# Kernel optimization log

Measured on AMD Instinct MI355X. Metric: run time of the kernel, lower is better.

Reference implementation:

```python
import jax, jax.numpy as jnp
import numpy as np

B = 8          # number of subgraphs (seq_start_end rows)
N = 2048       # nodes per subgraph (equal-size segments)
D = 64         # h_dim
H = 4          # gat_heads
ALPHA = 0.2    # leaky relu slope


def setup_inputs() -> dict:
    key = jax.random.key(0)
    k1, k2, k3, k4, k5 = jax.random.split(key, 5)
    h_states = jax.random.normal(k1, (B * N, D), dtype=jnp.float32)
    # xavier-ish scales
    W_heads = jax.random.normal(k2, (H, D, D), dtype=jnp.float32) * (1.414 * np.sqrt(2.0 / (D + D)))
    a_heads = jax.random.normal(k3, (H, 2 * D), dtype=jnp.float32) * (1.414 * np.sqrt(2.0 / (2 * D + 1)))
    W_out = jax.random.normal(k4, (H * D, D), dtype=jnp.float32) * (1.414 * np.sqrt(2.0 / (H * D + D)))
    a_out = jax.random.normal(k5, (2 * D,), dtype=jnp.float32) * (1.414 * np.sqrt(2.0 / (2 * D + 1)))
    starts = jnp.arange(B, dtype=jnp.int32) * N
    seq_start_end = jnp.stack([starts, starts + N], axis=1)  # (B, 2)
    return {"h_states": h_states, "W_heads": W_heads, "a_heads": a_heads,
            "W_out": W_out, "a_out": a_out, "seq_start_end": seq_start_end}


def _gat_layer(x, W, a):
    """Dense GAT layer. Equivalent to the torch.cat O(N^2*2d) construction,
    rewritten as separate a1/a2 projections + broadcast add. Eval mode (no dropout)."""
    h = x @ W                      # (N, dout)
    d = W.shape[1]
    s1 = h @ a[:d]                 # (N,)  score contribution of source node i
    s2 = h @ a[d:]                 # (N,)  score contribution of target node j
    e = jax.nn.leaky_relu(s1[:, None] + s2[None, :], ALPHA)  # (N, N)
    attn = jax.nn.softmax(e, axis=1)
    return attn @ h                # (N, dout)


def reference(h_states, W_heads, a_heads, W_out, a_out, seq_start_end):
    # seq_start_end encodes B equal contiguous segments of length N -> reshape
    x = h_states.reshape(B, N, D)

    def per_graph(xg):  # xg: (N, D)
        # multi-head attention layers, concat=True -> elu on each head output
        hp = jax.vmap(lambda W, a: jax.nn.elu(_gat_layer(xg, W, a)))(W_heads, a_heads)  # (H, N, D)
        xc = jnp.transpose(hp, (1, 0, 2)).reshape(N, H * D)
        # output attention layer, concat=False (no elu inside), then elu + log_softmax outside
        out = jax.nn.elu(_gat_layer(xc, W_out, a_out))   # (N, D)
        return jax.nn.log_softmax(out, axis=1)

    return jax.vmap(per_graph)(x).reshape(B * N, D)
```

## Files before the change

### kernel.cpp

```cpp
#include <hip/hip_runtime.h>
#include <math.h>

#define NTOT 16384
#define NSEG 2048
#define TROW 65
#define TSTRIDE 133185ull

#define OFF_HH   0ull
#define OFF_XC   4194304ull
#define OFF_S1H  8388608ull
#define OFF_S2H  8454144ull
#define OFF_S1O  8519680ull
#define OFF_S2O  8536064ull
#define OFF_SVAL 8552448ull
#define OFF_WN   8617984ull
#define OFF_CHA  8683520ull
#define OFF_CHS  8949760ull
#define OFF_SIDX 9216000ull
#define OFF_A    9281536ull
#define OFF_S    13543456ull

__device__ inline unsigned long long pack_key(float v, int idx) {
    unsigned u = __float_as_uint(v);
    u = (u & 0x80000000u) ? ~u : (u | 0x80000000u);
    return ((unsigned long long)u << 32) | (unsigned)idx;
}
__device__ inline float unpack_key(unsigned long long k) {
    unsigned u = (unsigned)(k >> 32);
    u = (u & 0x80000000u) ? (u ^ 0x80000000u) : ~u;
    return __uint_as_float(u);
}
__device__ inline unsigned long long shfl_xor_u64(unsigned long long x, int mask) {
    unsigned lo = (unsigned)x, hi = (unsigned)(x >> 32);
    lo = (unsigned)__shfl_xor((int)lo, mask, 64);
    hi = (unsigned)__shfl_xor((int)hi, mask, 64);
    return ((unsigned long long)hi << 32) | lo;
}

__global__ __launch_bounds__(256) void gemm1_k(const float* __restrict__ X,
                                               const float* __restrict__ Wh,
                                               const float* __restrict__ aH,
                                               float* __restrict__ hh,
                                               float* __restrict__ s1h,
                                               float* __restrict__ s2h) {
    __shared__ float As[64][68];
    __shared__ float Bs[64][68];
    const int tid = threadIdx.x;
    const int bm = blockIdx.x, h = blockIdx.y;
    const int c0 = tid & 63, r0 = tid >> 6;
#pragma unroll
    for (int r = 0; r < 16; ++r) {
        int row = r0 + r * 4;
        As[c0][row] = X[(size_t)(bm * 64 + row) * 64 + c0];
        Bs[row][c0] = Wh[h * 4096 + row * 64 + c0];
    }
    __syncthreads();
    const int tx = tid & 15, ty = tid >> 4;
    const int m0 = ty * 4, n0 = tx * 4;
    float acc[4][4] = {};
#pragma unroll
    for (int kk = 0; kk < 64; ++kk) {
        float4 a = *(const float4*)&As[kk][m0];
        float4 b = *(const float4*)&Bs[kk][n0];
        acc[0][0] += a.x * b.x; acc[0][1] += a.x * b.y; acc[0][2] += a.x * b.z; acc[0][3] += a.x * b.w;
        acc[1][0] += a.y * b.x; acc[1][1] += a.y * b.y; acc[1][2] += a.y * b.z; acc[1][3] += a.y * b.w;
        acc[2][0] += a.z * b.x; acc[2][1] += a.z * b.y; acc[2][2] += a.z * b.z; acc[2][3] += a.z * b.w;
        acc[3][0] += a.w * b.x; acc[3][1] += a.w * b.y; acc[3][2] += a.w * b.z; acc[3][3] += a.w * b.w;
    }
#pragma unroll
    for (int i = 0; i < 4; ++i) {
        float4 v = make_float4(acc[i][0], acc[i][1], acc[i][2], acc[i][3]);
        *(float4*)&hh[(size_t)(bm * 64 + m0 + i) * 256 + h * 64 + n0] = v;
    }
#pragma unroll
    for (int i = 0; i < 4; ++i) {
        float p1 = 0.f, p2 = 0.f;
#pragma unroll
        for (int jj = 0; jj < 4; ++jj) {
            p1 += acc[i][jj] * aH[h * 128 + n0 + jj];
            p2 += acc[i][jj] * aH[h * 128 + 64 + n0 + jj];
        }
#pragma unroll
        for (int off = 8; off; off >>= 1) {
            p1 += __shfl_xor(p1, off, 16);
            p2 += __shfl_xor(p2, off, 16);
        }
        if (tx == 0) {
            s1h[h * NTOT + bm * 64 + m0 + i] = p1;
            s2h[h * NTOT + bm * 64 + m0 + i] = p2;
        }
    }
}

__global__ __launch_bounds__(256) void gemm2_k(const float* __restrict__ XC,
                                               const float* __restrict__ Wo,
                                               const float* __restrict__ aO,
                                               float* __restrict__ hc,
                                               float* __restrict__ s1o,
                                               float* __restrict__ s2o) {
    __shared__ float As[64][68];
    __shared__ float Bs[64][68];
    const int tid = threadIdx.x;
    const int bm = blockIdx.x;
    const int c0 = tid & 63, r0 = tid >> 6;
    const int tx = tid & 15, ty = tid >> 4;
    const int m0 = ty * 4, n0 = tx * 4;
    float acc[4][4] = {};
    for (int kt = 0; kt < 4; ++kt) {
#pragma unroll
        for (int r = 0; r < 16; ++r) {
            int row = r0 + r * 4;
            As[c0][row] = XC[(size_t)(bm * 64 + row) * 256 + kt * 64 + c0];
            Bs[row][c0] = Wo[(kt * 64 + row) * 64 + c0];
        }
        __syncthreads();
#pragma unroll
        for (int kk = 0; kk < 64; ++kk) {
            float4 a = *(const float4*)&As[kk][m0];
            float4 b = *(const float4*)&Bs[kk][n0];
            acc[0][0] += a.x * b.x; acc[0][1] += a.x * b.y; acc[0][2] += a.x * b.z; acc[0][3] += a.x * b.w;
            acc[1][0] += a.y * b.x; acc[1][1] += a.y * b.y; acc[1][2] += a.y * b.z; acc[1][3] += a.y * b.w;
            acc[2][0] += a.z * b.x; acc[2][1] += a.z * b.y; acc[2][2] += a.z * b.z; acc[2][3] += a.z * b.w;
            acc[3][0] += a.w * b.x; acc[3][1] += a.w * b.y; acc[3][2] += a.w * b.z; acc[3][3] += a.w * b.w;
        }
        __syncthreads();
    }
#pragma unroll
    for (int i = 0; i < 4; ++i) {
        float4 v = make_float4(acc[i][0], acc[i][1], acc[i][2], acc[i][3]);
        *(float4*)&hc[(size_t)(bm * 64 + m0 + i) * 64 + n0] = v;
    }
#pragma unroll
    for (int i = 0; i < 4; ++i) {
        float p1 = 0.f, p2 = 0.f;
#pragma unroll
        for (int jj = 0; jj < 4; ++jj) {
            p1 += acc[i][jj] * aO[n0 + jj];
            p2 += acc[i][jj] * aO[64 + n0 + jj];
        }
#pragma unroll
        for (int off = 8; off; off >>= 1) {
            p1 += __shfl_xor(p1, off, 16);
            p2 += __shfl_xor(p2, off, 16);
        }
        if (tx == 0) {
            s1o[bm * 64 + m0 + i] = p1;
            s2o[bm * 64 + m0 + i] = p2;
        }
    }
}

__global__ __launch_bounds__(1024) void sort_k(const float* __restrict__ s2_all, int heads,
                                               float* __restrict__ g_sval, int* __restrict__ g_sidx,
                                               float* __restrict__ g_wN) {
    __shared__ unsigned long long sA[1024];
    __shared__ unsigned long long sB[1024];
    __shared__ float sM2;
    const int tid = threadIdx.x, t = blockIdx.x;
    const int g = t / heads, h = t % heads;
    const float* s2p = s2_all + (size_t)h * NTOT + (size_t)g * NSEG;
    unsigned long long a0 = pack_key(s2p[tid], tid);
    unsigned long long a1 = pack_key(s2p[tid + 1024], tid + 1024);
    for (int k = 2; k <= 2048; k <<= 1) {
        const bool up0 = (tid & k) == 0;
        const bool up1 = (((tid + 1024) & k) == 0);
        for (int j = k >> 1; j > 0; j >>= 1) {
            if (j >= 1024) {
                unsigned long long lo = a0 < a1 ? a0 : a1;
                unsigned long long hi = a0 < a1 ? a1 : a0;
                a0 = up0 ? lo : hi;
                a1 = up0 ? hi : lo;
            } else if (j >= 64) {
                __syncthreads();
                sA[tid] = a0; sB[tid] = a1;
                __syncthreads();
                unsigned long long p0 = sA[tid ^ j], p1 = sB[tid ^ j];
                bool lower = (tid & j) == 0;
                a0 = ((a0 < p0) == (lower == up0)) ? a0 : p0;
                a1 = ((a1 < p1) == (lower == up1)) ? a1 : p1;
            } else {
                unsigned long long p0 = shfl_xor_u64(a0, j);
                unsigned long long p1 = shfl_xor_u64(a1, j);
                bool lower = (tid & j) == 0;
                a0 = ((a0 < p0) == (lower == up0)) ? a0 : p0;
                a1 = ((a1 < p1) == (lower == up1)) ? a1 : p1;
            }
        }
    }
    float v0 = unpack_key(a0), v1 = unpack_key(a1);
    if (tid == 1023) sM2 = v1;
    __syncthreads();
    const float M2 = sM2;
    size_t o = (size_t)t * NSEG;
    g_sval[o + tid] = v0;
    g_sval[o + tid + 1024] = v1;
    g_sidx[o + tid] = (int)(unsigned)(a0 & 0xffffffffu);
    g_sidx[o + tid + 1024] = (int)(unsigned)(a1 & 0xffffffffu);
    g_wN[o + tid] = __expf(0.2f * (v0 - M2));
    g_wN[o + tid + 1024] = __expf(0.2f * (v1 - M2));
}

__global__ __launch_bounds__(256) void chunks_k(const float* __restrict__ V,
                                                int heads, int vstride,
                                                const int* __restrict__ g_sidx,
                                                const float* __restrict__ g_wN,
                                                float* __restrict__ g_chA, float* __restrict__ g_chS) {
    const int t = blockIdx.y, g = t / heads, h = t % heads;
    const int wv = threadIdx.x >> 6, lane = threadIdx.x & 63;
    const int c = blockIdx.x * 4 + wv, base = c * 16;
    const float* Vp = V + (size_t)g * NSEG * vstride + h * 64;
    float wn_l = 0.f; int si_l = 0;
    if (lane < 16) {
        wn_l = g_wN[(size_t)t * NSEG + base + lane];
        si_l = g_sidx[(size_t)t * NSEG + base + lane];
    }
    float sa = 0.f, swa = 0.f, ss = 0.f, sws = 0.f;
#pragma unroll
    for (int j = 0; j < 16; ++j) {
        float wn = __shfl(wn_l, j, 64);
        int row = __shfl(si_l, j, 64);
        float v = Vp[(size_t)row * vstride + lane];
        float w2 = wn * wn, wp = w2 * w2 * wn;
        sa += wn * v; swa += wn;
        ss += wp * v; sws += wp;
    }
    size_t o = ((size_t)t * 128 + c) * TROW;
    g_chA[o + lane] = sa;
    g_chS[o + lane] = ss;
    if (lane == 0) { g_chA[o + 64] = swa; g_chS[o + 64] = sws; }
}

__global__ __launch_bounds__(256) void scan_k(float* __restrict__ g_chA, float* __restrict__ g_chS,
                                              float* __restrict__ g_A, float* __restrict__ g_S) {
    __shared__ float M[128 * 65];
    const int t = blockIdx.x, tid = threadIdx.x;
    for (int i = tid; i < 8320; i += 256) M[i] = g_chA[(size_t)t * 8320 + i];
    __syncthreads();
    if (tid < 65) {
        float run = 0.f;
        for (int c = 0; c < 128; ++c) { float v = M[c * 65 + tid]; M[c * 65 + tid] = run; run += v; }
        g_A[(size_t)t * TSTRIDE + (size_t)2048 * TROW + tid] = run;
    }
    __syncthreads();
    for (int i = tid; i < 8320; i += 256) g_chA[(size_t)t * 8320 + i] = M[i];
    __syncthreads();
    for (int i = tid; i < 8320; i += 256) M[i] = g_chS[(size_t)t * 8320 + i];
    __syncthreads();
    if (tid < 65) {
        float run = 0.f;
        for (int c = 127; c >= 0; --c) { run += M[c * 65 + tid]; M[c * 65 + tid] = run; }
        g_S[(size_t)t * TSTRIDE + (size_t)2048 * TROW + tid] = 0.f;
    }
    __syncthreads();
    for (int i = tid; i < 8320; i += 256) g_chS[(size_t)t * 8320 + i] = M[i];
}

__global__ __launch_bounds__(256) void seg_tab_k(const float* __restrict__ V,
                                                 int heads, int vstride,
                                                 const int* __restrict__ g_sidx,
                                                 const float* __restrict__ g_wN,
                                                 const float* __restrict__ g_chA,
                                                 const float* __restrict__ g_chS,
                                                 float* __restrict__ g_A, float* __restrict__ g_S) {
    const int t = blockIdx.y, g = t / heads, h = t % heads;
    const int wv = threadIdx.x >> 6, lane = threadIdx.x & 63;
    const int c = blockIdx.x * 4 + wv;
    const int base = c * 16;
    const float* Vp = V + (size_t)g * NSEG * vstride + h * 64;
    const int* sidx = g_sidx + (size_t)t * NSEG + base;
    const float* wnp = g_wN + (size_t)t * NSEG + base;
    float wn[16], vv[16];
#pragma unroll
    for (int j = 0; j < 16; ++j) wn[j] = wnp[j];
#pragma unroll
    for (int j = 0; j < 16; ++j) vv[j] = Vp[(size_t)sidx[j] * vstride + lane];
    float* A = g_A + (size_t)t * TSTRIDE;
    float* S = g_S + (size_t)t * TSTRIDE;
    float accA = g_chA[((size_t)t * 128 + c) * TROW + lane];
    float scaA = g_chA[((size_t)t * 128 + c) * TROW + 64];
#pragma unroll
    for (int j = 0; j < 16; ++j) {
        size_t pos = base + j;
        A[pos * TROW + lane] = accA;
        if (lane == 0) A[pos * TROW + 64] = scaA;
        accA += wn[j] * vv[j]; scaA += wn[j];
    }
    float accS = 0.f, scaS = 0.f;
    if (c < 127) {
        accS = g_chS[((size_t)t * 128 + c + 1) * TROW + lane];
        scaS = g_chS[((size_t)t * 128 + c + 1) * TROW + 64];
    }
#pragma unroll
    for (int j = 15; j >= 0; --j) {
        float w = wn[j], w2 = w * w, wp = w2 * w2 * w;
        accS += wp * vv[j]; scaS += wp;
        size_t pos = base + j;
        S[pos * TROW + lane] = accS;
        if (lane == 0) S[pos * TROW + 64] = scaS;
    }
}

template <int MODE>
__global__ __launch_bounds__(256) void seg_query_k(const float* __restrict__ s1_all,
                                                   float* __restrict__ out,
                                                   int heads, int ostride,
                                                   const float* __restrict__ g_sval,
                                                   const float* __restrict__ g_A,
                                                   const float* __restrict__ g_S) {
    __shared__ float sval[NSEG];
    const int tid = threadIdx.x;
    const int t = blockIdx.y, g = t / heads, h = t % heads;
    const float4* sv4 = (const float4*)(g_sval + (size_t)t * NSEG);
    for (int i = tid; i < NSEG / 4; i += 256) ((float4*)sval)[i] = sv4[i];
    __syncthreads();
    const float M2 = sval[NSEG - 1];
    const int lane = tid & 63, wv = tid >> 6;
    const int q0 = blockIdx.x * 128 + wv * 32;
    const float* s1p = s1_all + (size_t)h * NTOT + (size_t)g * NSEG;
    float* outp = out + (size_t)g * NSEG * ostride + h * 64;
    const float* A = g_A + (size_t)t * TSTRIDE;
    const float* S = g_S + (size_t)t * TSTRIDE;
    int myq = q0 + (lane & 31);
    float s1v = s1p[myq];
    float th = -s1v;
    int lo = 0, hi = NSEG;
    while (lo < hi) { int mid = (lo + hi) >> 1; if (sval[mid] <= th) lo = mid + 1; else hi = mid; }
    for (int j = 0; j < 32; ++j) {
        int k = __shfl(lo, j, 64);
        float s1q = __shfl(s1v, j, 64);
        const float* rowA = A + (size_t)k * TROW;
        const float* rowS = S + (size_t)k * TROW;
        float accA = rowA[lane], scaA = rowA[64];
        float accS = rowS[lane], scaS = rowS[64];
        float cc = __expf(-0.8f * fmaxf(s1q + M2, 0.f));
        float o = (accS + cc * accA) / (scaS + cc * scaA);
        o = o > 0.f ? o : expm1f(o);
        int q = q0 + j;
        if (MODE == 0) {
            outp[(size_t)q * ostride + lane] = o;
        } else {
            float m = o;
#pragma unroll
            for (int off = 32; off; off >>= 1) m = fmaxf(m, __shfl_xor(m, off, 64));
            float e = __expf(o - m);
#pragma unroll
            for (int off = 32; off; off >>= 1) e += __shfl_xor(e, off, 64);
            outp[(size_t)q * ostride + lane] = o - m - __logf(e);
        }
    }
}

extern "C" void kernel_launch(void* const* d_in, const int* in_sizes, int n_in,
                              void* d_out, int out_size, void* d_ws, size_t ws_size,
                              hipStream_t stream) {
    const float* h_states = (const float*)d_in[0];
    const float* W_heads = (const float*)d_in[1];
    const float* a_heads = (const float*)d_in[2];
    const float* W_out = (const float*)d_in[3];
    const float* a_out = (const float*)d_in[4];
    float* w = (float*)d_ws;
    float* hh = w + OFF_HH;
    float* xc = w + OFF_XC;
    float* hc = w + OFF_HH;
    float* s1h = w + OFF_S1H;
    float* s2h = w + OFF_S2H;
    float* s1o = w + OFF_S1O;
    float* s2o = w + OFF_S2O;
    float* g_sval = w + OFF_SVAL;
    float* g_wN = w + OFF_WN;
    float* g_chA = w + OFF_CHA;
    float* g_chS = w + OFF_CHS;
    int* g_sidx = (int*)(w + OFF_SIDX);
    float* g_A = w + OFF_A;
    float* g_S = w + OFF_S;
    float* outp = (float*)d_out;

    gemm1_k<<<dim3(256, 4), 256, 0, stream>>>(h_states, W_heads, a_heads, hh, s1h, s2h);
    sort_k<<<32, 1024, 0, stream>>>(s2h, 4, g_sval, g_sidx, g_wN);
    chunks_k<<<dim3(32, 32), 256, 0, stream>>>(hh, 4, 256, g_sidx, g_wN, g_chA, g_chS);
    scan_k<<<32, 256, 0, stream>>>(g_chA, g_chS, g_A, g_S);
    seg_tab_k<<<dim3(32, 32), 256, 0, stream>>>(hh, 4, 256, g_sidx, g_wN, g_chA, g_chS, g_A, g_S);
    seg_query_k<0><<<dim3(16, 32), 256, 0, stream>>>(s1h, xc, 4, 256, g_sval, g_A, g_S);
    gemm2_k<<<256, 256, 0, stream>>>(xc, W_out, a_out, hc, s1o, s2o);
    sort_k<<<8, 1024, 0, stream>>>(s2o, 1, g_sval, g_sidx, g_wN);
    chunks_k<<<dim3(32, 8), 256, 0, stream>>>(hc, 1, 64, g_sidx, g_wN, g_chA, g_chS);
    scan_k<<<8, 256, 0, stream>>>(g_chA, g_chS, g_A, g_S);
    seg_tab_k<<<dim3(32, 8), 256, 0, stream>>>(hc, 1, 64, g_sidx, g_wN, g_chA, g_chS, g_A, g_S);
    seg_query_k<1><<<dim3(16, 8), 256, 0, stream>>>(s1o, outp, 1, 64, g_sval, g_A, g_S);
}
```

Measured before the change: 211.4 us.

## Fuse sort, chunk reduction and scan into one kernel; halve queries per block

Merges the bitonic sort, the per-chunk weighted sums and the chunk prefix scan into a single 1024-thread block per (graph, head). Sorted indices and weights stay in shared memory, and the scan runs as a two-level blocked scan in LDS. This removes two kernel launches and a global round trip of the chunk tables. The trade-off is only 32 (or 8) blocks doing the chunk gathers, which lowers parallelism for that phase. Separately, the query kernel now handles 16 queries per wave instead of 32 with twice as many blocks, to raise occupancy.

```diff
diff --git a/kernel.cpp b/kernel.cpp
--- a/kernel.cpp
+++ b/kernel.cpp
@@ -150,15 +150,27 @@
     }
 }
 
-__global__ __launch_bounds__(1024) void sort_k(const float* __restrict__ s2_all, int heads,
-                                               float* __restrict__ g_sval, int* __restrict__ g_sidx,
-                                               float* __restrict__ g_wN) {
+__global__ __launch_bounds__(1024) void sortchunkscan_k(const float* __restrict__ s2_all,
+                                                        const float* __restrict__ V,
+                                                        int heads, int vstride,
+                                                        float* __restrict__ g_sval, int* __restrict__ g_sidx,
+                                                        float* __restrict__ g_wN,
+                                                        float* __restrict__ g_chA, float* __restrict__ g_chS,
+                                                        float* __restrict__ g_A, float* __restrict__ g_S) {
     __shared__ unsigned long long sA[1024];
     __shared__ unsigned long long sB[1024];
+    __shared__ float chA[8320];
+    __shared__ float chS[8320];
+    __shared__ float swn[NSEG];
+    __shared__ int ssi[NSEG];
+    __shared__ float btA[4][65];
+    __shared__ float btS[4][65];
     __shared__ float sM2;
     const int tid = threadIdx.x, t = blockIdx.x;
     const int g = t / heads, h = t % heads;
     const float* s2p = s2_all + (size_t)h * NTOT + (size_t)g * NSEG;
+    const float* Vp = V + (size_t)g * NSEG * vstride + h * 64;
+
     unsigned long long a0 = pack_key(s2p[tid], tid);
     unsigned long long a1 = pack_key(s2p[tid + 1024], tid + 1024);
     for (int k = 2; k <= 2048; k <<= 1) {
@@ -191,68 +203,68 @@
     if (tid == 1023) sM2 = v1;
     __syncthreads();
     const float M2 = sM2;
+    int i0 = (int)(unsigned)(a0 & 0xffffffffu);
+    int i1 = (int)(unsigned)(a1 & 0xffffffffu);
+    float w0 = __expf(0.2f * (v0 - M2));
+    float w1 = __expf(0.2f * (v1 - M2));
     size_t o = (size_t)t * NSEG;
-    g_sval[o + tid] = v0;
-    g_sval[o + tid + 1024] = v1;
-    g_sidx[o + tid] = (int)(unsigned)(a0 & 0xffffffffu);
-    g_sidx[o + tid + 1024] = (int)(unsigned)(a1 & 0xffffffffu);
-    g_wN[o + tid] = __expf(0.2f * (v0 - M2));
-    g_wN[o + tid + 1024] = __expf(0.2f * (v1 - M2));
-}
-
-__global__ __launch_bounds__(256) void chunks_k(const float* __restrict__ V,
-                                                int heads, int vstride,
-                                                const int* __restrict__ g_sidx,
-                                                const float* __restrict__ g_wN,
-                                                float* __restrict__ g_chA, float* __restrict__ g_chS) {
-    const int t = blockIdx.y, g = t / heads, h = t % heads;
-    const int wv = threadIdx.x >> 6, lane = threadIdx.x & 63;
-    const int c = blockIdx.x * 4 + wv, base = c * 16;
-    const float* Vp = V + (size_t)g * NSEG * vstride + h * 64;
-    float wn_l = 0.f; int si_l = 0;
-    if (lane < 16) {
-        wn_l = g_wN[(size_t)t * NSEG + base + lane];
-        si_l = g_sidx[(size_t)t * NSEG + base + lane];
-    }
-    float sa = 0.f, swa = 0.f, ss = 0.f, sws = 0.f;
-#pragma unroll
-    for (int j = 0; j < 16; ++j) {
-        float wn = __shfl(wn_l, j, 64);
-        int row = __shfl(si_l, j, 64);
-        float v = Vp[(size_t)row * vstride + lane];
-        float w2 = wn * wn, wp = w2 * w2 * wn;
-        sa += wn * v; swa += wn;
-        ss += wp * v; sws += wp;
-    }
-    size_t o = ((size_t)t * 128 + c) * TROW;
-    g_chA[o + lane] = sa;
-    g_chS[o + lane] = ss;
-    if (lane == 0) { g_chA[o + 64] = swa; g_chS[o + 64] = sws; }
-}
-
-__global__ __launch_bounds__(256) void scan_k(float* __restrict__ g_chA, float* __restrict__ g_chS,
-                                              float* __restrict__ g_A, float* __restrict__ g_S) {
-    __shared__ float M[128 * 65];
-    const int t = blockIdx.x, tid = threadIdx.x;
-    for (int i = tid; i < 8320; i += 256) M[i] = g_chA[(size_t)t * 8320 + i];
+    g_sval[o + tid] = v0; g_sval[o + tid + 1024] = v1;
+    g_sidx[o + tid] = i0; g_sidx[o + tid + 1024] = i1;
+    g_wN[o + tid] = w0;   g_wN[o + tid + 1024] = w1;
+    swn[tid] = w0; swn[tid + 1024] = w1;
+    ssi[tid] = i0; ssi[tid + 1024] = i1;
+    __syncthreads();
+    const int wv = tid >> 6, lane = tid & 63;
+    for (int cc = 0; cc < 8; ++cc) {
+        int c = wv * 8 + cc, base = c * 16;
+        float sa = 0.f, swa = 0.f, ss = 0.f, sws = 0.f;
+#pragma unroll
+        for (int j = 0; j < 16; ++j) {
+            float wn = swn[base + j];
+            int row = ssi[base + j];
+            float v = Vp[(size_t)row * vstride + lane];
+            float w2 = wn * wn, wp = w2 * w2 * wn;
+            sa += wn * v; swa += wn;
+            ss += wp * v; sws += wp;
+        }
+        chA[c * 65 + lane] = sa; chS[c * 65 + lane] = ss;
+        if (lane == 0) { chA[c * 65 + 64] = swa; chS[c * 65 + 64] = sws; }
+    }
+    __syncthreads();
+    if (tid < 260) {
+        int b = tid / 65, d = tid % 65;
+        float run = 0.f;
+        for (int c = b * 32; c < b * 32 + 32; ++c) { float v = chA[c * 65 + d]; chA[c * 65 + d] = run; run += v; }
+        btA[b][d] = run;
+    } else if (tid >= 512 && tid < 772) {
+        int u = tid - 512;
+        int b = u / 65, d = u % 65;
+        float run = 0.f;
+        for (int c = b * 32 + 31; c >= b * 32; --c) { run += chS[c * 65 + d]; chS[c * 65 + d] = run; }
+        btS[b][d] = run;
+    }
     __syncthreads();
     if (tid < 65) {
         float run = 0.f;
-        for (int c = 0; c < 128; ++c) { float v = M[c * 65 + tid]; M[c * 65 + tid] = run; run += v; }
+        for (int b = 0; b < 4; ++b) { float v = btA[b][tid]; btA[b][tid] = run; run += v; }
         g_A[(size_t)t * TSTRIDE + (size_t)2048 * TROW + tid] = run;
-    }
-    __syncthreads();
-    for (int i = tid; i < 8320; i += 256) g_chA[(size_t)t * 8320 + i] = M[i];
-    __syncthreads();
-    for (int i = tid; i < 8320; i += 256) M[i] = g_chS[(size_t)t * 8320 + i];
-    __syncthreads();
-    if (tid < 65) {
+    } else if (tid >= 512 && tid < 577) {
+        int d = tid - 512;
         float run = 0.f;
-        for (int c = 127; c >= 0; --c) { run += M[c * 65 + tid]; M[c * 65 + tid] = run; }
-        g_S[(size_t)t * TSTRIDE + (size_t)2048 * TROW + tid] = 0.f;
-    }
-    __syncthreads();
-    for (int i = tid; i < 8320; i += 256) g_chS[(size_t)t * 8320 + i] = M[i];
+        for (int b = 3; b >= 0; --b) { float v = btS[b][d]; btS[b][d] = run; run += v; }
+        g_S[(size_t)t * TSTRIDE + (size_t)2048 * TROW + d] = 0.f;
+    }
+    __syncthreads();
+    if (tid < 512) {
+        for (int i = tid; i < 8320; i += 512) chA[i] += btA[(i / 65) >> 5][i % 65];
+    } else {
+        for (int i = tid - 512; i < 8320; i += 512) chS[i] += btS[(i / 65) >> 5][i % 65];
+    }
+    __syncthreads();
+    for (int i = tid; i < 8320; i += 1024) {
+        g_chA[(size_t)t * 8320 + i] = chA[i];
+        g_chS[(size_t)t * 8320 + i] = chS[i];
+    }
 }
 
 __global__ __launch_bounds__(256) void seg_tab_k(const float* __restrict__ V,
@@ -315,17 +327,17 @@
     __syncthreads();
     const float M2 = sval[NSEG - 1];
     const int lane = tid & 63, wv = tid >> 6;
-    const int q0 = blockIdx.x * 128 + wv * 32;
+    const int q0 = blockIdx.x * 64 + wv * 16;
     const float* s1p = s1_all + (size_t)h * NTOT + (size_t)g * NSEG;
     float* outp = out + (size_t)g * NSEG * ostride + h * 64;
     const float* A = g_A + (size_t)t * TSTRIDE;
     const float* S = g_S + (size_t)t * TSTRIDE;
-    int myq = q0 + (lane & 31);
+    int myq = q0 + (lane & 15);
     float s1v = s1p[myq];
     float th = -s1v;
     int lo = 0, hi = NSEG;
     while (lo < hi) { int mid = (lo + hi) >> 1; if (sval[mid] <= th) lo = mid + 1; else hi = mid; }
-    for (int j = 0; j < 32; ++j) {
+    for (int j = 0; j < 16; ++j) {
         int k = __shfl(lo, j, 64);
         float s1q = __shfl(s1v, j, 64);
         const float* rowA = A + (size_t)k * TROW;
@@ -376,15 +388,11 @@
     float* outp = (float*)d_out;
 
     gemm1_k<<<dim3(256, 4), 256, 0, stream>>>(h_states, W_heads, a_heads, hh, s1h, s2h);
-    sort_k<<<32, 1024, 0, stream>>>(s2h, 4, g_sval, g_sidx, g_wN);
-    chunks_k<<<dim3(32, 32), 256, 0, stream>>>(hh, 4, 256, g_sidx, g_wN, g_chA, g_chS);
-    scan_k<<<32, 256, 0, stream>>>(g_chA, g_chS, g_A, g_S);
+    sortchunkscan_k<<<32, 1024, 0, stream>>>(s2h, hh, 4, 256, g_sval, g_sidx, g_wN, g_chA, g_chS, g_A, g_S);
     seg_tab_k<<<dim3(32, 32), 256, 0, stream>>>(hh, 4, 256, g_sidx, g_wN, g_chA, g_chS, g_A, g_S);
-    seg_query_k<0><<<dim3(16, 32), 256, 0, stream>>>(s1h, xc, 4, 256, g_sval, g_A, g_S);
+    seg_query_k<0><<<dim3(32, 32), 256, 0, stream>>>(s1h, xc, 4, 256, g_sval, g_A, g_S);
     gemm2_k<<<256, 256, 0, stream>>>(xc, W_out, a_out, hc, s1o, s2o);
-    sort_k<<<8, 1024, 0, stream>>>(s2o, 1, g_sval, g_sidx, g_wN);
-    chunks_k<<<dim3(32, 8), 256, 0, stream>>>(hc, 1, 64, g_sidx, g_wN, g_chA, g_chS);
-    scan_k<<<8, 256, 0, stream>>>(g_chA, g_chS, g_A, g_S);
+    sortchunkscan_k<<<8, 1024, 0, stream>>>(s2o, hc, 1, 64, g_sval, g_sidx, g_wN, g_chA, g_chS, g_A, g_S);
     seg_tab_k<<<dim3(32, 8), 256, 0, stream>>>(hc, 1, 64, g_sidx, g_wN, g_chA, g_chS, g_A, g_S);
-    seg_query_k<1><<<dim3(16, 8), 256, 0, stream>>>(s1o, outp, 1, 64, g_sval, g_A, g_S);
-}
+    seg_query_k<1><<<dim3(32, 8), 256, 0, stream>>>(s1o, outp, 1, 64, g_sval, g_A, g_S);
+}
```

After: 203.7 us. -3.7%, faster.
